# Optimization experiments

Measured on AMD Instinct MI355X. Metric: run time of the kernel, lower is better.

## Reference

```python
import jax, jax.numpy as jnp
import numpy as np

H = 16; W = 16; C_IN = 32; RNN_IN = 64; HID = 128; OUT = 512; B = 512


def _upsample_bilinear_ac(x, oh, ow):
    """Bilinear upsample with align_corners=True (matches nn.UpsamplingBilinear2d). x: (B,C,h,w)."""
    h, w = x.shape[2], x.shape[3]
    ys = (jnp.arange(oh, dtype=jnp.float32) * (h - 1) / (oh - 1))
    y0 = jnp.floor(ys).astype(jnp.int32)
    y1 = jnp.minimum(y0 + 1, h - 1)
    wy = (ys - y0.astype(jnp.float32))[None, None, :, None]
    xs = (jnp.arange(ow, dtype=jnp.float32) * (w - 1) / (ow - 1))
    x0 = jnp.floor(xs).astype(jnp.int32)
    x1 = jnp.minimum(x0 + 1, w - 1)
    wx = (xs - x0.astype(jnp.float32))[None, None, None, :]
    rows = x[:, :, y0, :] * (1.0 - wy) + x[:, :, y1, :] * wy  # (B,C,oh,w)
    out = rows[:, :, :, x0] * (1.0 - wx) + rows[:, :, :, x1] * wx  # (B,C,oh,ow)
    return out


def setup_inputs() -> dict:
    key = jax.random.key(0)
    ks = jax.random.split(key, 8)
    def winit(k, shape, fan_in):
        return jax.random.normal(k, shape, jnp.float32) / np.float32(np.sqrt(fan_in))
    return {
        "x": jax.random.normal(ks[0], (B, C_IN, H, W), jnp.float32),
        "h0": jax.random.normal(ks[1], (B, HID), jnp.float32),
        "W_in": winit(ks[2], (RNN_IN, C_IN), C_IN),
        "b_in": jnp.zeros((RNN_IN,), jnp.float32),
        "W_ih": winit(ks[3], (HID, RNN_IN), RNN_IN),
        "b_ih": jnp.zeros((HID,), jnp.float32),
        "W_hh": winit(ks[4], (HID, HID), HID),
        "b_hh": jnp.zeros((HID,), jnp.float32),
        "W_out": winit(ks[5], (OUT, HID), HID),
        "b_out": jnp.zeros((OUT,), jnp.float32),
    }


def reference(x, h0, W_in, b_in, W_ih, b_ih, W_hh, b_hh, W_out, b_out):
    b = x.shape[0]
    # (B,C,H,W) -> (B,L,C), L = H*W raster order
    x_seq = x.transpose(0, 2, 3, 1).reshape(b, H * W, C_IN)
    proj = x_seq @ W_in.T + b_in                      # (B,L,RNN_IN)
    pre = proj @ W_ih.T + b_ih                        # (B,L,HID), input part of RNNCell precomputed

    def step(h, p_t):
        h_new = jnp.tanh(p_t + h @ W_hh.T + b_hh)
        return h_new, h_new

    _, hs = jax.lax.scan(step, h0, pre.transpose(1, 0, 2))  # (L,B,HID)
    hs_map = hs.reshape(H, W, b, HID).transpose(2, 3, 0, 1)  # (B,HID,H,W)
    up = _upsample_bilinear_ac(hs_map, 2 * H, 2 * W)         # (B,HID,32,32)
    act = up * jnp.clip(up + 3.0, 0.0, 6.0) * (1.0 / 6.0)    # hardswish
    pooled = act.mean(axis=(2, 3))                           # (B,HID)
    return pooled @ W_out.T + b_out
```

## Files before the change

kernel.cpp:

```cpp
#include <hip/hip_runtime.h>

#define L 256
#define BATCH 512
#define CIN 32
#define HIDN 128
#define OUTN 512

typedef _Float16 f16x8 __attribute__((ext_vector_type(8)));
typedef float f32x4 __attribute__((ext_vector_type(4)));

#define MFMA16(a, b, c) __builtin_amdgcn_mfma_f32_16x16x32_f16(a, b, c, 0, 0, 0)

static __device__ __forceinline__ unsigned short f16b(_Float16 h) {
    unsigned short u; __builtin_memcpy(&u, &h, 2); return u;
}


__global__ __launch_bounds__(256) void prep_kernel(
    const float* __restrict__ W_in, const float* __restrict__ b_in,
    const float* __restrict__ W_ih, const float* __restrict__ b_ih,
    const float* __restrict__ b_hh, const float* __restrict__ Whh,
    unsigned short* __restrict__ Wh, unsigned short* __restrict__ Wl,
    unsigned short* __restrict__ Wch, unsigned short* __restrict__ Wcl,
    float* __restrict__ bpre)
{
    const int tid = threadIdx.x;
    __shared__ float win[64 * CIN];
    for (int i = tid; i < 64 * CIN; i += 256) win[i] = W_in[i];
    __syncthreads();
    if (tid < 128) {
        const int j = tid;
        float acc[CIN];
#pragma unroll
        for (int c = 0; c < CIN; ++c) acc[c] = 0.f;
        float bs = b_ih[j] + b_hh[j];
        for (int m = 0; m < 64; ++m) {
            float w = W_ih[j * 64 + m];
            bs += w * b_in[m];
#pragma unroll
            for (int c = 0; c < CIN; ++c) acc[c] += w * win[m * CIN + c];
        }
        bpre[j] = bs;
#pragma unroll
        for (int c = 0; c < CIN; ++c) {
            _Float16 h = (_Float16)acc[c];
            _Float16 l = (_Float16)(acc[c] - (float)h);
            Wch[j * CIN + c] = f16b(h);
            Wcl[j * CIN + c] = f16b(l);
        }
    } else {
        const int j = tid - 128;
        for (int k = 0; k < HIDN; k += 4) {
            float4 v = *(const float4*)(Whh + j * HIDN + k);
            float vv[4] = {v.x, v.y, v.z, v.w};
#pragma unroll
            for (int u = 0; u < 4; ++u) {
                _Float16 h = (_Float16)vv[u];
                _Float16 l = (_Float16)(vv[u] - (float)h);
                Wh[j * HIDN + k + u] = f16b(h);
                Wl[j * HIDN + k + u] = f16b(l);
            }
        }
    }
}

__global__ __launch_bounds__(512, 1) void rnn_kernel(
    const float* __restrict__ x, const float* __restrict__ h0,
    const unsigned short* __restrict__ Wh, const unsigned short* __restrict__ Wl,
    const unsigned short* __restrict__ Wch, const unsigned short* __restrict__ Wcl,
    const float* __restrict__ bpre, unsigned short* __restrict__ hs)
{
    const int tid = threadIdx.x;
    const int bb = blockIdx.x;
    const int lane = tid & 63;
    const int w = tid >> 6;
    const int n = lane & 15;
    const int q = lane >> 4;

    __shared__ unsigned short hbuf[2][16][HIDN];
    __shared__ unsigned short xcl[2][16][64][8];

    f16x8 Ah[4], Al[4], Axh, Axl;
    const int jr = w * 16 + n;
#pragma unroll
    for (int kc = 0; kc < 4; ++kc) {
        Ah[kc] = *(const f16x8*)(Wh + jr * HIDN + kc * 32 + q * 8);
        Al[kc] = *(const f16x8*)(Wl + jr * HIDN + kc * 32 + q * 8);
    }
    Axh = *(const f16x8*)(Wch + jr * CIN + q * 8);
    Axl = *(const f16x8*)(Wcl + jr * CIN + q * 8);
    float4 bv = *(const float4*)(bpre + w * 16 + q * 4);
    f32x4 bp = (f32x4){bv.x, bv.y, bv.z, bv.w};
    const f32x4 zero4 = (f32x4){0.f, 0.f, 0.f, 0.f};

    if (tid < 256) {
        const int ni = tid >> 4, gi = tid & 15;
        const float4* src = (const float4*)(h0 + ((size_t)bb * 16 + ni) * HIDN + gi * 8);
        float4 a = src[0], b4 = src[1];
        float vv[8] = {a.x, a.y, a.z, a.w, b4.x, b4.y, b4.z, b4.w};
        unsigned short o[8];
#pragma unroll
        for (int i = 0; i < 8; ++i) o[i] = f16b((_Float16)vv[i]);
        *(uint4*)&hbuf[0][ni][(gi ^ (ni & 7)) * 8] = *(uint4*)o;
    }

    float4 xr[4];
    auto issue_chunk = [&](int ci) {
#pragma unroll
        for (int r = 0; r < 4; ++r) {
            int i = tid + r * 512;
            int nn = i >> 7, cc = (i >> 2) & 31, tq = i & 3;
            xr[r] = *(const float4*)(x + (((size_t)bb * 16 + nn) * CIN + cc) * L + ci * 16 + tq * 4);
        }
    };
    auto write_chunk = [&](int buf) {
#pragma unroll
        for (int r = 0; r < 4; ++r) {
            int i = tid + r * 512;
            int nn = i >> 7, cc = (i >> 2) & 31, tq = i & 3;
            int gr = (cc >> 3) * 16 + (nn ^ ((cc >> 3) << 2));
            float vv[4] = {xr[r].x, xr[r].y, xr[r].z, xr[r].w};
#pragma unroll
            for (int k = 0; k < 4; ++k)
                xcl[buf][tq * 4 + k][gr][cc & 7] = f16b((_Float16)vv[k]);
        }
    };

    issue_chunk(0);
    write_chunk(0);
    issue_chunk(1);
    __syncthreads();

    unsigned short* hsp = hs + ((size_t)bb * 16 + n) * HIDN + w * 16 + q * 4;
    const int G = (w * 2 + (q >> 1)) ^ (n & 7);
    const int sw = n & 7;
    const int grs = q * 16 + (n ^ (q << 2));

    f16x8 xb0, xb1;
    xb0 = *(const f16x8*)&xcl[0][0][grs][0];

#define STEP(T, IN, OUT, OFF, XCUR, XNEXT)                                     \
    {                                                                          \
        f16x8 Bh0 = *(const f16x8*)&hbuf[IN][n][((0 + q) ^ sw) * 8];           \
        f16x8 Bh1 = *(const f16x8*)&hbuf[IN][n][((4 + q) ^ sw) * 8];           \
        f16x8 Bh2 = *(const f16x8*)&hbuf[IN][n][((8 + q) ^ sw) * 8];           \
        f16x8 Bh3 = *(const f16x8*)&hbuf[IN][n][((12 + q) ^ sw) * 8];          \
        f32x4 c0 = MFMA16(Axh, XCUR, bp);            \
        f32x4 c2 = MFMA16(Axl, XCUR, zero4);                                   \
        c0 = MFMA16(Ah[0], Bh0, c0);                                           \
        c2 = MFMA16(Al[0], Bh0, c2);                                           \
        f32x4 c1 = MFMA16(Ah[1], Bh1, zero4);                                  \
        f32x4 c3 = MFMA16(Al[1], Bh1, zero4);                                  \
        c0 = MFMA16(Ah[2], Bh2, c0);                                           \
        c2 = MFMA16(Al[2], Bh2, c2);                                           \
        c1 = MFMA16(Ah[3], Bh3, c1);                                           \
        c3 = MFMA16(Al[3], Bh3, c3);                                           \
        if (((T) & 15) == 14 && (T) < L - 16) {                                \
            write_chunk((((T) >> 4) & 1) ^ 1);                                 \
            if ((T) < L - 32) issue_chunk(((T) >> 4) + 2);                     \
        }                                                                      \
        f32x4 acc = (c0 + c1) + (c2 + c3);                                     \
        unsigned short o[4];                                                   \
        for (int r = 0; r < 4; ++r) {                                          \
            float e = __expf(2.f * acc[r]);                                    \
            float hv = 1.f - 2.f * __builtin_amdgcn_rcpf(e + 1.f);             \
            o[r] = f16b((_Float16)hv);                                         \
        }                                                                      \
        uint2 pk; __builtin_memcpy(&pk, o, 8);                                 \
        *(uint2*)&hbuf[OUT][n][G * 8 + (q & 1) * 4] = pk;                      \
        *(uint2*)(hsp + (OFF)) = pk;                                           \
        XNEXT = *(const f16x8*)&xcl[(((T) + 1) >> 4) & 1][((T) + 1) & 15][grs][0]; \
        asm volatile("" ::: "memory");                                         \
        __builtin_amdgcn_s_waitcnt(0xC17F);   \
        __builtin_amdgcn_s_barrier();         \
        asm volatile("" ::: "memory");                                         \
    }

    for (int t = 0; t < L; t += 2) {
        STEP(t,     0, 1, 0,             xb0, xb1);
        STEP(t + 1, 1, 0, BATCH * HIDN,  xb1, xb0);
        hsp += 2 * (BATCH * HIDN);
    }
#undef STEP
}

__global__ __launch_bounds__(256) void pool_out_kernel(
    const unsigned short* __restrict__ hs, const float* __restrict__ W_out,
    const float* __restrict__ b_out, float* __restrict__ out)
{
    const int b = blockIdx.x, tid = threadIdx.x;
    __shared__ unsigned short m[L][HIDN];
    __shared__ float ps[2][HIDN];
    __shared__ float pooled_s[HIDN];

#pragma unroll
    for (int it = 0; it < 16; ++it) {
        int i = tid + it * 256;
        int t = i >> 4, g = i & 15;
        *(uint4*)&m[t][g * 8] =
            *(const uint4*)(hs + (size_t)t * (BATCH * HIDN) + b * HIDN + g * 8);
    }
    __syncthreads();

    const int jo = tid & 127, sub = tid >> 7;
    float acc = 0.f;
    for (int oy = sub * 16; oy < sub * 16 + 16; ++oy) {
        float ysf = oy * (15.f / 31.f);
        int y0 = (int)ysf; float wy = ysf - (float)y0; int y1 = min(y0 + 1, 15);
        float rb[16];
#pragma unroll
        for (int sx = 0; sx < 16; ++sx) {
            float v0 = (float)*(const _Float16*)&m[y0 * 16 + sx][jo];
            float v1 = (float)*(const _Float16*)&m[y1 * 16 + sx][jo];
            rb[sx] = v0 + wy * (v1 - v0);
        }
#pragma unroll
        for (int ox = 0; ox < 32; ++ox) {
            float xsf = ox * (15.f / 31.f);
            int x0 = (int)xsf; float wx = xsf - (float)x0; int x1 = min(x0 + 1, 15);
            float v = rb[x0] + wx * (rb[x1] - rb[x0]);
            float t6 = fminf(fmaxf(v + 3.f, 0.f), 6.f);
            acc += v * t6;
        }
    }
    ps[sub][jo] = acc;
    __syncthreads();
    if (tid < 128) pooled_s[tid] = (ps[0][tid] + ps[1][tid]) * (1.f / 6144.f);
    __syncthreads();

    for (int o = tid; o < OUTN; o += 256) {
        float a = b_out[o];
#pragma unroll 8
        for (int k = 0; k < HIDN; k += 4) {
            float4 wv = *(const float4*)(W_out + o * HIDN + k);
            float4 pv = *(const float4*)&pooled_s[k];
            a += wv.x * pv.x + wv.y * pv.y + wv.z * pv.z + wv.w * pv.w;
        }
        out[b * OUTN + o] = a;
    }
}

extern "C" void kernel_launch(void* const* d_in, const int* in_sizes, int n_in,
                              void* d_out, int out_size, void* d_ws, size_t ws_size,
                              hipStream_t stream)
{
    const float* x     = (const float*)d_in[0];
    const float* h0    = (const float*)d_in[1];
    const float* W_in  = (const float*)d_in[2];
    const float* b_in  = (const float*)d_in[3];
    const float* W_ih  = (const float*)d_in[4];
    const float* b_ih  = (const float*)d_in[5];
    const float* W_hh  = (const float*)d_in[6];
    const float* b_hh  = (const float*)d_in[7];
    const float* W_out = (const float*)d_in[8];
    const float* b_out = (const float*)d_in[9];
    float* out = (float*)d_out;

    char* wsb = (char*)d_ws;
    unsigned short* Wh  = (unsigned short*)(wsb);
    unsigned short* Wl  = (unsigned short*)(wsb + 32768);
    unsigned short* Wch = (unsigned short*)(wsb + 65536);
    unsigned short* Wcl = (unsigned short*)(wsb + 73728);
    float* bpre         = (float*)(wsb + 81920);
    unsigned short* hsb = (unsigned short*)(wsb + 98304);

    prep_kernel<<<1, 256, 0, stream>>>(W_in, b_in, W_ih, b_ih, b_hh, W_hh,
                                       Wh, Wl, Wch, Wcl, bpre);
    rnn_kernel<<<32, 512, 0, stream>>>(x, h0, Wh, Wl, Wch, Wcl, bpre, hsb);
    pool_out_kernel<<<512, 256, 0, stream>>>(hsb, W_out, b_out, out);
}
```

Before: 217.1 us.

## Process 32 batch rows per RNN block with two j-tiles per wave

Each RNN block now handles 32 batch columns instead of 16, launching 16 blocks instead of 32. Each wave computes two 16-row hidden tiles for 16 of the columns, so every B-fragment load from LDS feeds twice as many MFMAs and the serial per-step barrier is shared across more work. The x staging layout is changed to match the wider tile, and prep_kernel stages W_ih and b_in in shared memory. The cost is fewer active CUs and roughly twice the MFMA and tanh work per step on the serial critical path, plus higher register pressure.

```diff
diff --git a/kernel.cpp b/kernel.cpp
--- a/kernel.cpp
+++ b/kernel.cpp
@@ -26,7 +26,11 @@
 {
     const int tid = threadIdx.x;
     __shared__ float win[64 * CIN];
+    __shared__ float wih[128 * 64];
+    __shared__ float binS[64];
     for (int i = tid; i < 64 * CIN; i += 256) win[i] = W_in[i];
+    for (int i = tid; i < 128 * 64; i += 256) wih[i] = W_ih[i];
+    if (tid < 64) binS[tid] = b_in[tid];
     __syncthreads();
     if (tid < 128) {
         const int j = tid;
@@ -35,8 +39,8 @@
         for (int c = 0; c < CIN; ++c) acc[c] = 0.f;
         float bs = b_ih[j] + b_hh[j];
         for (int m = 0; m < 64; ++m) {
-            float w = W_ih[j * 64 + m];
-            bs += w * b_in[m];
+            float w = wih[j * 64 + m];
+            bs += w * binS[m];
 #pragma unroll
             for (int c = 0; c < CIN; ++c) acc[c] += w * win[m * CIN + c];
         }
@@ -44,9 +48,9 @@
 #pragma unroll
         for (int c = 0; c < CIN; ++c) {
             _Float16 h = (_Float16)acc[c];
-            _Float16 l = (_Float16)(acc[c] - (float)h);
+            _Float16 lo = (_Float16)(acc[c] - (float)h);
             Wch[j * CIN + c] = f16b(h);
-            Wcl[j * CIN + c] = f16b(l);
+            Wcl[j * CIN + c] = f16b(lo);
         }
     } else {
         const int j = tid - 128;
@@ -56,15 +60,15 @@
 #pragma unroll
             for (int u = 0; u < 4; ++u) {
                 _Float16 h = (_Float16)vv[u];
-                _Float16 l = (_Float16)(vv[u] - (float)h);
+                _Float16 lo = (_Float16)(vv[u] - (float)h);
                 Wh[j * HIDN + k + u] = f16b(h);
-                Wl[j * HIDN + k + u] = f16b(l);
+                Wl[j * HIDN + k + u] = f16b(lo);
             }
         }
     }
 }
 
-__global__ __launch_bounds__(512, 1) void rnn_kernel(
+__global__ __launch_bounds__(512, 2) void rnn_kernel(
     const float* __restrict__ x, const float* __restrict__ h0,
     const unsigned short* __restrict__ Wh, const unsigned short* __restrict__ Wl,
     const unsigned short* __restrict__ Wch, const unsigned short* __restrict__ Wcl,
@@ -74,28 +78,36 @@
     const int bb = blockIdx.x;
     const int lane = tid & 63;
     const int w = tid >> 6;
-    const int n = lane & 15;
+    const int jg = w >> 1;
+    const int nh = w & 1;
+    const int nl = lane & 15;
     const int q = lane >> 4;
-
-    __shared__ unsigned short hbuf[2][16][HIDN];
-    __shared__ unsigned short xcl[2][16][64][8];
-
-    f16x8 Ah[4], Al[4], Axh, Axl;
-    const int jr = w * 16 + n;
-#pragma unroll
-    for (int kc = 0; kc < 4; ++kc) {
-        Ah[kc] = *(const f16x8*)(Wh + jr * HIDN + kc * 32 + q * 8);
-        Al[kc] = *(const f16x8*)(Wl + jr * HIDN + kc * 32 + q * 8);
-    }
-    Axh = *(const f16x8*)(Wch + jr * CIN + q * 8);
-    Axl = *(const f16x8*)(Wcl + jr * CIN + q * 8);
-    float4 bv = *(const float4*)(bpre + w * 16 + q * 4);
-    f32x4 bp = (f32x4){bv.x, bv.y, bv.z, bv.w};
+    const int n = nh * 16 + nl;
+
+    __shared__ unsigned short hbuf[2][32][HIDN];
+    __shared__ unsigned short xcl[2][16][32][CIN];
+
+    f16x8 Ah[2][4], Al[2][4], Axh[2], Axl[2];
+#pragma unroll
+    for (int jt = 0; jt < 2; ++jt) {
+        const int jr = jg * 32 + jt * 16 + nl;
+#pragma unroll
+        for (int kc = 0; kc < 4; ++kc) {
+            Ah[jt][kc] = *(const f16x8*)(Wh + jr * HIDN + kc * 32 + q * 8);
+            Al[jt][kc] = *(const f16x8*)(Wl + jr * HIDN + kc * 32 + q * 8);
+        }
+        Axh[jt] = *(const f16x8*)(Wch + jr * CIN + q * 8);
+        Axl[jt] = *(const f16x8*)(Wcl + jr * CIN + q * 8);
+    }
+    float4 bv0 = *(const float4*)(bpre + jg * 32 + q * 4);
+    float4 bv1 = *(const float4*)(bpre + jg * 32 + 16 + q * 4);
+    f32x4 bp0 = (f32x4){bv0.x, bv0.y, bv0.z, bv0.w};
+    f32x4 bp1 = (f32x4){bv1.x, bv1.y, bv1.z, bv1.w};
     const f32x4 zero4 = (f32x4){0.f, 0.f, 0.f, 0.f};
 
-    if (tid < 256) {
+    {
         const int ni = tid >> 4, gi = tid & 15;
-        const float4* src = (const float4*)(h0 + ((size_t)bb * 16 + ni) * HIDN + gi * 8);
+        const float4* src = (const float4*)(h0 + ((size_t)bb * 32 + ni) * HIDN + gi * 8);
         float4 a = src[0], b4 = src[1];
         float vv[8] = {a.x, a.y, a.z, a.w, b4.x, b4.y, b4.z, b4.w};
         unsigned short o[8];
@@ -104,25 +116,25 @@
         *(uint4*)&hbuf[0][ni][(gi ^ (ni & 7)) * 8] = *(uint4*)o;
     }
 
-    float4 xr[4];
+    float4 xr[8];
     auto issue_chunk = [&](int ci) {
 #pragma unroll
-        for (int r = 0; r < 4; ++r) {
+        for (int r = 0; r < 8; ++r) {
             int i = tid + r * 512;
             int nn = i >> 7, cc = (i >> 2) & 31, tq = i & 3;
-            xr[r] = *(const float4*)(x + (((size_t)bb * 16 + nn) * CIN + cc) * L + ci * 16 + tq * 4);
+            xr[r] = *(const float4*)(x + (((size_t)bb * 32 + nn) * CIN + cc) * L + ci * 16 + tq * 4);
         }
     };
     auto write_chunk = [&](int buf) {
 #pragma unroll
-        for (int r = 0; r < 4; ++r) {
+        for (int r = 0; r < 8; ++r) {
             int i = tid + r * 512;
             int nn = i >> 7, cc = (i >> 2) & 31, tq = i & 3;
-            int gr = (cc >> 3) * 16 + (nn ^ ((cc >> 3) << 2));
+            int cidx = (cc & 7) + 8 * ((cc >> 3) ^ (nn & 3));
             float vv[4] = {xr[r].x, xr[r].y, xr[r].z, xr[r].w};
 #pragma unroll
             for (int k = 0; k < 4; ++k)
-                xcl[buf][tq * 4 + k][gr][cc & 7] = f16b((_Float16)vv[k]);
+                xcl[buf][tq * 4 + k][nn][cidx] = f16b((_Float16)vv[k]);
         }
     };
 
@@ -131,13 +143,14 @@
     issue_chunk(1);
     __syncthreads();
 
-    unsigned short* hsp = hs + ((size_t)bb * 16 + n) * HIDN + w * 16 + q * 4;
-    const int G = (w * 2 + (q >> 1)) ^ (n & 7);
+    unsigned short* hsp = hs + ((size_t)bb * 32 + n) * HIDN + jg * 32 + q * 4;
     const int sw = n & 7;
-    const int grs = q * 16 + (n ^ (q << 2));
+    const int grsx = (q ^ (n & 3)) * 8;
+    const int G0 = ((jg * 4 + 0 + (q >> 1)) ^ sw) * 8 + (q & 1) * 4;
+    const int G1 = ((jg * 4 + 2 + (q >> 1)) ^ sw) * 8 + (q & 1) * 4;
 
     f16x8 xb0, xb1;
-    xb0 = *(const f16x8*)&xcl[0][0][grs][0];
+    xb0 = *(const f16x8*)&xcl[0][0][n][grsx];
 
 #define STEP(T, IN, OUT, OFF, XCUR, XNEXT)                                     \
     {                                                                          \
@@ -145,31 +158,49 @@
         f16x8 Bh1 = *(const f16x8*)&hbuf[IN][n][((4 + q) ^ sw) * 8];           \
         f16x8 Bh2 = *(const f16x8*)&hbuf[IN][n][((8 + q) ^ sw) * 8];           \
         f16x8 Bh3 = *(const f16x8*)&hbuf[IN][n][((12 + q) ^ sw) * 8];          \
-        f32x4 c0 = MFMA16(Axh, XCUR, bp);            \
-        f32x4 c2 = MFMA16(Axl, XCUR, zero4);                                   \
-        c0 = MFMA16(Ah[0], Bh0, c0);                                           \
-        c2 = MFMA16(Al[0], Bh0, c2);                                           \
-        f32x4 c1 = MFMA16(Ah[1], Bh1, zero4);                                  \
-        f32x4 c3 = MFMA16(Al[1], Bh1, zero4);                                  \
-        c0 = MFMA16(Ah[2], Bh2, c0);                                           \
-        c2 = MFMA16(Al[2], Bh2, c2);                                           \
-        c1 = MFMA16(Ah[3], Bh3, c1);                                           \
-        c3 = MFMA16(Al[3], Bh3, c3);                                           \
+        f32x4 c0 = MFMA16(Axh[0], XCUR, bp0);        \
+        f32x4 c2 = MFMA16(Axl[0], XCUR, zero4);                                \
+        f32x4 d0 = MFMA16(Axh[1], XCUR, bp1);                                  \
+        f32x4 d2 = MFMA16(Axl[1], XCUR, zero4);                                \
+        c0 = MFMA16(Ah[0][0], Bh0, c0);                                        \
+        c2 = MFMA16(Al[0][0], Bh0, c2);                                        \
+        d0 = MFMA16(Ah[1][0], Bh0, d0);                                        \
+        d2 = MFMA16(Al[1][0], Bh0, d2);                                        \
+        c0 = MFMA16(Ah[0][1], Bh1, c0);                                        \
+        c2 = MFMA16(Al[0][1], Bh1, c2);                                        \
+        d0 = MFMA16(Ah[1][1], Bh1, d0);                                        \
+        d2 = MFMA16(Al[1][1], Bh1, d2);                                        \
+        c0 = MFMA16(Ah[0][2], Bh2, c0);                                        \
+        c2 = MFMA16(Al[0][2], Bh2, c2);                                        \
+        d0 = MFMA16(Ah[1][2], Bh2, d0);                                        \
+        d2 = MFMA16(Al[1][2], Bh2, d2);                                        \
+        c0 = MFMA16(Ah[0][3], Bh3, c0);                                        \
+        c2 = MFMA16(Al[0][3], Bh3, c2);                                        \
+        d0 = MFMA16(Ah[1][3], Bh3, d0);                                        \
+        d2 = MFMA16(Al[1][3], Bh3, d2);                                        \
         if (((T) & 15) == 14 && (T) < L - 16) {                                \
             write_chunk((((T) >> 4) & 1) ^ 1);                                 \
             if ((T) < L - 32) issue_chunk(((T) >> 4) + 2);                     \
         }                                                                      \
-        f32x4 acc = (c0 + c1) + (c2 + c3);                                     \
-        unsigned short o[4];                                                   \
+        f32x4 acc0 = c0 + c2;                                                  \
+        f32x4 acc1 = d0 + d2;                                                  \
+        unsigned short o0[4], o1[4];                                           \
         for (int r = 0; r < 4; ++r) {                                          \
-            float e = __expf(2.f * acc[r]);                                    \
-            float hv = 1.f - 2.f * __builtin_amdgcn_rcpf(e + 1.f);             \
-            o[r] = f16b((_Float16)hv);                                         \
+            float e0 = __expf(2.f * acc0[r]);                                  \
+            float h0v = 1.f - 2.f * __builtin_amdgcn_rcpf(e0 + 1.f);           \
+            o0[r] = f16b((_Float16)h0v);                                       \
+            float e1 = __expf(2.f * acc1[r]);                                  \
+            float h1v = 1.f - 2.f * __builtin_amdgcn_rcpf(e1 + 1.f);           \
+            o1[r] = f16b((_Float16)h1v);                                       \
         }                                                                      \
-        uint2 pk; __builtin_memcpy(&pk, o, 8);                                 \
-        *(uint2*)&hbuf[OUT][n][G * 8 + (q & 1) * 4] = pk;                      \
-        *(uint2*)(hsp + (OFF)) = pk;                                           \
-        XNEXT = *(const f16x8*)&xcl[(((T) + 1) >> 4) & 1][((T) + 1) & 15][grs][0]; \
+        uint2 pk0, pk1;                                                        \
+        __builtin_memcpy(&pk0, o0, 8);                                         \
+        __builtin_memcpy(&pk1, o1, 8);                                         \
+        *(uint2*)&hbuf[OUT][n][G0] = pk0;                                      \
+        *(uint2*)&hbuf[OUT][n][G1] = pk1;                                      \
+        *(uint2*)(hsp + (OFF)) = pk0;                                          \
+        *(uint2*)(hsp + (OFF) + 16) = pk1;                                     \
+        XNEXT = *(const f16x8*)&xcl[(((T) + 1) >> 4) & 1][((T) + 1) & 15][n][grsx]; \
         asm volatile("" ::: "memory");                                         \
         __builtin_amdgcn_s_waitcnt(0xC17F);   \
         __builtin_amdgcn_s_barrier();         \
@@ -266,6 +297,6 @@
 
     prep_kernel<<<1, 256, 0, stream>>>(W_in, b_in, W_ih, b_ih, b_hh, W_hh,
                                        Wh, Wl, Wch, Wcl, bpre);
-    rnn_kernel<<<32, 512, 0, stream>>>(x, h0, Wh, Wl, Wch, Wcl, bpre, hsb);
+    rnn_kernel<<<16, 512, 0, stream>>>(x, h0, Wh, Wl, Wch, Wcl, bpre, hsb);
     pool_out_kernel<<<512, 256, 0, stream>>>(hsb, W_out, b_out, out);
 }
```

After: 300.0 us. 1.38x slower.

## Fuse weight preparation into RNN kernel and break MFMA accumulation chains

Applied to the files above, without the earlier changes.

Removes the separate single-block prep kernel and has each RNN block compute its own fp16 hi/lo split of W_hh and the combined W_ih·W_in weights and bias from shared memory. This drops one kernel launch and a serial dependency on a slow one-block kernel, at the cost of redundant prologue work in each of the 32 blocks. The per-step MFMA chain is also rewritten into ten independent accumulators summed at the end, shortening the dependent MFMA latency chain on the serial recurrence critical path while using more registers.

```diff
diff --git a/kernel.cpp b/kernel.cpp
--- a/kernel.cpp
+++ b/kernel.cpp
@@ -16,59 +16,12 @@
 }
 
 
-__global__ __launch_bounds__(256) void prep_kernel(
+__global__ __launch_bounds__(512, 1) void rnn_kernel(
+    const float* __restrict__ x, const float* __restrict__ h0,
     const float* __restrict__ W_in, const float* __restrict__ b_in,
     const float* __restrict__ W_ih, const float* __restrict__ b_ih,
-    const float* __restrict__ b_hh, const float* __restrict__ Whh,
-    unsigned short* __restrict__ Wh, unsigned short* __restrict__ Wl,
-    unsigned short* __restrict__ Wch, unsigned short* __restrict__ Wcl,
-    float* __restrict__ bpre)
-{
-    const int tid = threadIdx.x;
-    __shared__ float win[64 * CIN];
-    for (int i = tid; i < 64 * CIN; i += 256) win[i] = W_in[i];
-    __syncthreads();
-    if (tid < 128) {
-        const int j = tid;
-        float acc[CIN];
-#pragma unroll
-        for (int c = 0; c < CIN; ++c) acc[c] = 0.f;
-        float bs = b_ih[j] + b_hh[j];
-        for (int m = 0; m < 64; ++m) {
-            float w = W_ih[j * 64 + m];
-            bs += w * b_in[m];
-#pragma unroll
-            for (int c = 0; c < CIN; ++c) acc[c] += w * win[m * CIN + c];
-        }
-        bpre[j] = bs;
-#pragma unroll
-        for (int c = 0; c < CIN; ++c) {
-            _Float16 h = (_Float16)acc[c];
-            _Float16 l = (_Float16)(acc[c] - (float)h);
-            Wch[j * CIN + c] = f16b(h);
-            Wcl[j * CIN + c] = f16b(l);
-        }
-    } else {
-        const int j = tid - 128;
-        for (int k = 0; k < HIDN; k += 4) {
-            float4 v = *(const float4*)(Whh + j * HIDN + k);
-            float vv[4] = {v.x, v.y, v.z, v.w};
-#pragma unroll
-            for (int u = 0; u < 4; ++u) {
-                _Float16 h = (_Float16)vv[u];
-                _Float16 l = (_Float16)(vv[u] - (float)h);
-                Wh[j * HIDN + k + u] = f16b(h);
-                Wl[j * HIDN + k + u] = f16b(l);
-            }
-        }
-    }
-}
-
-__global__ __launch_bounds__(512, 1) void rnn_kernel(
-    const float* __restrict__ x, const float* __restrict__ h0,
-    const unsigned short* __restrict__ Wh, const unsigned short* __restrict__ Wl,
-    const unsigned short* __restrict__ Wch, const unsigned short* __restrict__ Wcl,
-    const float* __restrict__ bpre, unsigned short* __restrict__ hs)
+    const float* __restrict__ W_hh, const float* __restrict__ b_hh,
+    unsigned short* __restrict__ hs)
 {
     const int tid = threadIdx.x;
     const int bb = blockIdx.x;
@@ -79,19 +32,37 @@
 
     __shared__ unsigned short hbuf[2][16][HIDN];
     __shared__ unsigned short xcl[2][16][64][8];
-
-    f16x8 Ah[4], Al[4], Axh, Axl;
-    const int jr = w * 16 + n;
-#pragma unroll
-    for (int kc = 0; kc < 4; ++kc) {
-        Ah[kc] = *(const f16x8*)(Wh + jr * HIDN + kc * 32 + q * 8);
-        Al[kc] = *(const f16x8*)(Wl + jr * HIDN + kc * 32 + q * 8);
-    }
-    Axh = *(const f16x8*)(Wch + jr * CIN + q * 8);
-    Axl = *(const f16x8*)(Wcl + jr * CIN + q * 8);
-    float4 bv = *(const float4*)(bpre + w * 16 + q * 4);
-    f32x4 bp = (f32x4){bv.x, bv.y, bv.z, bv.w};
-    const f32x4 zero4 = (f32x4){0.f, 0.f, 0.f, 0.f};
+    __shared__ float wih_s[128][65];
+    __shared__ float win_s[64][32];
+    __shared__ float bin_s[64];
+
+    float4 xr[4];
+    auto issue_chunk = [&](int ci) {
+#pragma unroll
+        for (int r = 0; r < 4; ++r) {
+            int i = tid + r * 512;
+            int nn = i >> 7, cc = (i >> 2) & 31, tq = i & 3;
+            xr[r] = *(const float4*)(x + (((size_t)bb * 16 + nn) * CIN + cc) * L + ci * 16 + tq * 4);
+        }
+    };
+    auto write_chunk = [&](int buf) {
+#pragma unroll
+        for (int r = 0; r < 4; ++r) {
+            int i = tid + r * 512;
+            int nn = i >> 7, cc = (i >> 2) & 31, tq = i & 3;
+            int gr = (cc >> 3) * 16 + (nn ^ ((cc >> 3) << 2));
+            float vv[4] = {xr[r].x, xr[r].y, xr[r].z, xr[r].w};
+#pragma unroll
+            for (int k = 0; k < 4; ++k)
+                xcl[buf][tq * 4 + k][gr][cc & 7] = f16b((_Float16)vv[k]);
+        }
+    };
+
+    issue_chunk(0);
+
+    for (int i = tid; i < 128 * 64; i += 512) wih_s[i >> 6][i & 63] = W_ih[i];
+    for (int i = tid; i < 64 * 32; i += 512) ((float*)win_s)[i] = W_in[i];
+    if (tid < 64) bin_s[tid] = b_in[tid];
 
     if (tid < 256) {
         const int ni = tid >> 4, gi = tid & 15;
@@ -103,30 +74,53 @@
         for (int i = 0; i < 8; ++i) o[i] = f16b((_Float16)vv[i]);
         *(uint4*)&hbuf[0][ni][(gi ^ (ni & 7)) * 8] = *(uint4*)o;
     }
-
-    float4 xr[4];
-    auto issue_chunk = [&](int ci) {
-#pragma unroll
-        for (int r = 0; r < 4; ++r) {
-            int i = tid + r * 512;
-            int nn = i >> 7, cc = (i >> 2) & 31, tq = i & 3;
-            xr[r] = *(const float4*)(x + (((size_t)bb * 16 + nn) * CIN + cc) * L + ci * 16 + tq * 4);
-        }
-    };
-    auto write_chunk = [&](int buf) {
-#pragma unroll
-        for (int r = 0; r < 4; ++r) {
-            int i = tid + r * 512;
-            int nn = i >> 7, cc = (i >> 2) & 31, tq = i & 3;
-            int gr = (cc >> 3) * 16 + (nn ^ ((cc >> 3) << 2));
-            float vv[4] = {xr[r].x, xr[r].y, xr[r].z, xr[r].w};
-#pragma unroll
-            for (int k = 0; k < 4; ++k)
-                xcl[buf][tq * 4 + k][gr][cc & 7] = f16b((_Float16)vv[k]);
-        }
-    };
-
-    issue_chunk(0);
+    __syncthreads();
+
+    const int jr = w * 16 + n;
+    f16x8 Ah[4], Al[4];
+    const float* wrow = W_hh + jr * HIDN;
+#pragma unroll
+    for (int kc = 0; kc < 4; ++kc) {
+        float4 v0 = *(const float4*)(wrow + kc * 32 + q * 8);
+        float4 v1 = *(const float4*)(wrow + kc * 32 + q * 8 + 4);
+        float vv[8] = {v0.x, v0.y, v0.z, v0.w, v1.x, v1.y, v1.z, v1.w};
+        f16x8 H, Lo;
+#pragma unroll
+        for (int i = 0; i < 8; ++i) {
+            _Float16 hi = (_Float16)vv[i];
+            H[i] = hi;
+            Lo[i] = (_Float16)(vv[i] - (float)hi);
+        }
+        Ah[kc] = H; Al[kc] = Lo;
+    }
+    float acc8[8];
+#pragma unroll
+    for (int i = 0; i < 8; ++i) acc8[i] = 0.f;
+    for (int m = 0; m < 64; ++m) {
+        float wv = wih_s[jr][m];
+        const float* wc = &win_s[m][q * 8];
+#pragma unroll
+        for (int i = 0; i < 8; ++i) acc8[i] += wv * wc[i];
+    }
+    f16x8 Axh, Axl;
+#pragma unroll
+    for (int i = 0; i < 8; ++i) {
+        _Float16 hi = (_Float16)acc8[i];
+        Axh[i] = hi;
+        Axl[i] = (_Float16)(acc8[i] - (float)hi);
+    }
+    const int jb0 = w * 16 + q * 4;
+    float bs4[4];
+#pragma unroll
+    for (int r = 0; r < 4; ++r) bs4[r] = b_ih[jb0 + r] + b_hh[jb0 + r];
+    for (int m = 0; m < 64; ++m) {
+        float bm = bin_s[m];
+#pragma unroll
+        for (int r = 0; r < 4; ++r) bs4[r] += wih_s[jb0 + r][m] * bm;
+    }
+    f32x4 bp = (f32x4){bs4[0], bs4[1], bs4[2], bs4[3]};
+    const f32x4 zero4 = (f32x4){0.f, 0.f, 0.f, 0.f};
+
     write_chunk(0);
     issue_chunk(1);
     __syncthreads();
@@ -145,21 +139,22 @@
         f16x8 Bh1 = *(const f16x8*)&hbuf[IN][n][((4 + q) ^ sw) * 8];           \
         f16x8 Bh2 = *(const f16x8*)&hbuf[IN][n][((8 + q) ^ sw) * 8];           \
         f16x8 Bh3 = *(const f16x8*)&hbuf[IN][n][((12 + q) ^ sw) * 8];          \
-        f32x4 c0 = MFMA16(Axh, XCUR, bp);            \
-        f32x4 c2 = MFMA16(Axl, XCUR, zero4);                                   \
-        c0 = MFMA16(Ah[0], Bh0, c0);                                           \
-        c2 = MFMA16(Al[0], Bh0, c2);                                           \
-        f32x4 c1 = MFMA16(Ah[1], Bh1, zero4);                                  \
-        f32x4 c3 = MFMA16(Al[1], Bh1, zero4);                                  \
-        c0 = MFMA16(Ah[2], Bh2, c0);                                           \
-        c2 = MFMA16(Al[2], Bh2, c2);                                           \
-        c1 = MFMA16(Ah[3], Bh3, c1);                                           \
-        c3 = MFMA16(Al[3], Bh3, c3);                                           \
+        f32x4 c0 = MFMA16(Axh, XCUR, bp);              \
+        f32x4 d0 = MFMA16(Axl, XCUR, zero4);                                   \
+        f32x4 c1 = MFMA16(Ah[0], Bh0, zero4);                                  \
+        f32x4 d1 = MFMA16(Al[0], Bh0, zero4);                                  \
+        f32x4 c2 = MFMA16(Ah[1], Bh1, zero4);                                  \
+        f32x4 d2 = MFMA16(Al[1], Bh1, zero4);                                  \
+        f32x4 c3 = MFMA16(Ah[2], Bh2, zero4);                                  \
+        f32x4 d3 = MFMA16(Al[2], Bh2, zero4);                                  \
+        f32x4 c4 = MFMA16(Ah[3], Bh3, zero4);                                  \
+        f32x4 d4 = MFMA16(Al[3], Bh3, zero4);                                  \
         if (((T) & 15) == 14 && (T) < L - 16) {                                \
             write_chunk((((T) >> 4) & 1) ^ 1);                                 \
             if ((T) < L - 32) issue_chunk(((T) >> 4) + 2);                     \
         }                                                                      \
-        f32x4 acc = (c0 + c1) + (c2 + c3);                                     \
+        f32x4 acc = ((c0 + c1) + (c2 + c3)) +                                  \
+                    ((d0 + d1) + (d2 + d3)) + (c4 + d4);                       \
         unsigned short o[4];                                                   \
         for (int r = 0; r < 4; ++r) {                                          \
             float e = __expf(2.f * acc[r]);                                    \
@@ -256,16 +251,9 @@
     const float* b_out = (const float*)d_in[9];
     float* out = (float*)d_out;
 
-    char* wsb = (char*)d_ws;
-    unsigned short* Wh  = (unsigned short*)(wsb);
-    unsigned short* Wl  = (unsigned short*)(wsb + 32768);
-    unsigned short* Wch = (unsigned short*)(wsb + 65536);
-    unsigned short* Wcl = (unsigned short*)(wsb + 73728);
-    float* bpre         = (float*)(wsb + 81920);
-    unsigned short* hsb = (unsigned short*)(wsb + 98304);
-
-    prep_kernel<<<1, 256, 0, stream>>>(W_in, b_in, W_ih, b_ih, b_hh, W_hh,
-                                       Wh, Wl, Wch, Wcl, bpre);
-    rnn_kernel<<<32, 512, 0, stream>>>(x, h0, Wh, Wl, Wch, Wcl, bpre, hsb);
+    unsigned short* hsb = (unsigned short*)d_ws;
+
+    rnn_kernel<<<32, 512, 0, stream>>>(x, h0, W_in, b_in, W_ih, b_ih,
+                                       W_hh, b_hh, hsb);
     pool_out_kernel<<<512, 256, 0, stream>>>(hsb, W_out, b_out, out);
 }
```

After: 228.2 us. 5.1% more time.
